# Optimization experiments

Hardware: AMD Instinct MI355X
Metric: run time of the kernel (lower is better)

Reference implementation:

```python
import jax, jax.numpy as jnp
import numpy as np

WS = 8  # window_size

def conv2d(x, w, b, padding=0, dilation=1, groups=1):
    out = jax.lax.conv_general_dilated(
        x, w, window_strides=(1, 1),
        padding=[(padding, padding), (padding, padding)],
        rhs_dilation=(dilation, dilation),
        feature_group_count=groups)
    return out + b[None, :, None, None]

def lrelu(x):
    return jnp.where(x >= 0, x, 0.1 * x)

def ln_cf(x, w, b, eps=1e-6):
    # LayerNorm, channels_first: normalize over channel dim per pixel
    u = x.mean(1, keepdims=True)
    s = ((x - u) ** 2).mean(1, keepdims=True)
    x = (x - u) / jnp.sqrt(s + eps)
    return w[None, :, None, None] * x + b[None, :, None, None]

def window_part(x, ws):
    # b c (h dh) (w dw) -> b (h w) (dh dw c)
    b, c, H, W = x.shape
    h, w = H // ws, W // ws
    x = x.reshape(b, c, h, ws, w, ws).transpose(0, 2, 4, 3, 5, 1)
    return x.reshape(b, h * w, ws * ws * c)

def window_rev(x, ws, H, W, c):
    # b (h w) (dh dw c) -> b c (h dh) (w dw)
    b = x.shape[0]
    h, w = H // ws, W // ws
    x = x.reshape(b, h, w, ws, ws, c).transpose(0, 5, 1, 3, 2, 4)
    return x.reshape(b, c, H, W)

def setup_inputs() -> dict:
    key = jax.random.key(0)
    B, C, H, W = 4, 64, 256, 256
    ws = WS
    E = ws * ws * C  # 4096
    ks = iter(jax.random.split(key, 40))
    def rn(shape, scale=1.0):
        return jax.random.normal(next(ks), shape, jnp.float32) * scale
    z = lambda *s: jnp.zeros(s, jnp.float32)
    d = {}
    d['x'] = rn((B, C, H, W))
    d['Wv'] = rn((C, C, 1, 1), C ** -0.5); d['bv'] = z(C)
    d['Wri'] = rn((C // 4, C, 1, 1), C ** -0.5); d['bri'] = z(C // 4)
    d['Wrc'] = rn((C // 4, C, 1, 1), C ** -0.5); d['brc'] = z(C // 4)
    d['ln_w'] = jnp.ones((C // 4,), jnp.float32); d['ln_b'] = z(C // 4)
    d['Wca'] = rn((C, C // 4, 1, 1), (C // 4) ** -0.5); d['bca'] = z(C)
    d['Wsa'] = rn((1, C // 4, 3, 3), (9 * C // 4) ** -0.5); d['bsa'] = z(1)
    d['Wm1'] = rn((E // 2, E), E ** -0.5); d['bm1'] = z(E // 2)
    d['Wm2'] = rn((E, E // 2), (E // 2) ** -0.5); d['bm2'] = z(E)
    d['Wq'] = rn((C, C), C ** -0.5); d['bq'] = z(C)
    d['Wk'] = rn((C, C), C ** -0.5); d['bk'] = z(C)
    d['Wd1'] = rn((C, 1, 3, 3), 1.0 / 3.0); d['bd1'] = z(C)
    d['Wd2'] = rn((C, 1, 3, 3), 1.0 / 3.0); d['bd2'] = z(C)
    d['Wo'] = rn((C, C, 1, 1), C ** -0.5); d['bo'] = z(C)
    return d

def reference(x, Wv, bv, Wri, bri, Wrc, brc, ln_w, ln_b, Wca, bca, Wsa, bsa,
              Wm1, bm1, Wm2, bm2, Wq, bq, Wk, bk, Wd1, bd1, Wd2, bd2, Wo, bo):
    B, C, H, W = x.shape
    ws = WS
    E = ws * ws * C
    v = conv2d(x, Wv, bv)
    # ---- MaskPre (route) ----
    x1 = lrelu(conv2d(v, Wri, bri))                       # [B,C/4,H,W]
    x_ = lrelu(ln_cf(conv2d(v, Wrc, brc), ln_w, ln_b))    # [B,C/4,H,W]
    ca = jax.nn.sigmoid(conv2d(x_.mean((2, 3), keepdims=True), Wca, bca))  # [B,C,1,1]
    sa = jax.nn.sigmoid(conv2d(x_, Wsa, bsa, padding=1))                   # [B,1,H,W]
    xm = window_part(x1.mean(1, keepdims=True), ws)       # [B,N,ws^2]
    var_x = jnp.var(xm, axis=-1, ddof=1)                  # torch.var is unbiased
    N = var_x.shape[1]
    k_top = N // 2
    _, idx = jax.lax.top_k(-var_x, k_top)                 # k smallest-variance windows
    mask_bin = jnp.ones((B, N), x.dtype).at[jnp.arange(B)[:, None], idx].set(0.0)
    m = jnp.broadcast_to(mask_bin[:, :, None], (B, N, E))
    m = lrelu(m @ Wm1.T + bm1)
    mask = m @ Wm2.T + bm2                                # [B,N,E]
    # ---- windowed attention / skip split ----
    vs = v * sa
    vw = window_part(v, ws)                               # [B,N,ws^2*C]
    vsw = window_part(vs, ws)
    qkw = window_part(jnp.concatenate([x, x], axis=1), ws)  # [B,N,ws^2*2C]
    v1 = vw * mask
    v2 = vsw * (1.0 - mask)
    mask_qk = jnp.concatenate(
        [mask.reshape(B, N, ws * ws, C)] * 2, axis=-1).reshape(B, N, ws * ws * 2 * C)
    qk1 = (qkw * mask_qk).reshape(B, N * ws * ws, 2 * C)
    q1 = (qk1[..., :C] @ Wq.T + bq).reshape(B * N, ws * ws, C)
    k1 = (qk1[..., C:] @ Wk.T + bk).reshape(B * N, ws * ws, C)
    v1r = v1.reshape(B * N, ws * ws, C)
    attn = jax.nn.softmax(q1 @ jnp.swapaxes(k1, -1, -2), axis=-1)  # [BN,ws^2,ws^2]
    f_attn = (attn @ v1r).reshape(B, N, ws * ws * C)
    attn_out = f_attn + v2
    out = window_rev(attn_out, ws, H, W, C)               # [B,C,H,W]
    # ---- spatial conv branch + projections ----
    c1 = conv2d(out, Wd1, bd1, padding=1, groups=C)
    c2 = conv2d(c1, Wd2, bd2, padding=2, dilation=2, groups=C)
    out = jax.nn.gelu(c2, approximate=False) * ca + out
    out = conv2d(out, Wo, bo)
    return out
```

## Files before the change

### kernel.cpp

```cpp
#include <hip/hip_runtime.h>
#include <hip/hip_bf16.h>
#include <math.h>

typedef __attribute__((ext_vector_type(8))) short short8;
typedef __attribute__((ext_vector_type(16))) float f32x16;

__device__ __forceinline__ float lrelu(float x){ return x >= 0.f ? x : 0.1f*x; }
__device__ __forceinline__ float sigmoidf(float x){ return 1.f/(1.f+expf(-x)); }
__device__ __forceinline__ short f2bf(float f){
  __hip_bfloat16 hb = __float2bfloat16(f);
  return *reinterpret_cast<short*>(&hb);
}
__device__ __forceinline__ float bf16f(short s){
  return __uint_as_float(((unsigned)(unsigned short)s)<<16);
}

__global__ void k0_combine(const float* __restrict__ Wv, const float* __restrict__ bv,
                           const float* __restrict__ Wri, const float* __restrict__ bri,
                           const float* __restrict__ Wrc, const float* __restrict__ brc,
                           float* __restrict__ WriE, float* __restrict__ briE,
                           float* __restrict__ WrcE, float* __restrict__ brcE){
  int idx = blockIdx.x*256 + threadIdx.x;
  if (idx < 1024){
    int j = idx>>6, c = idx&63;
    float s1=0.f, s2=0.f;
    for (int k=0;k<64;k++){ s1 = fmaf(Wri[j*64+k], Wv[k*64+c], s1); s2 = fmaf(Wrc[j*64+k], Wv[k*64+c], s2); }
    WriE[idx]=s1; WrcE[idx]=s2;
  }
  if (idx < 16){
    float s1=bri[idx], s2=brc[idx];
    for (int k=0;k<64;k++){ s1 = fmaf(Wri[idx*64+k], bv[k], s1); s2 = fmaf(Wrc[idx*64+k], bv[k], s2); }
    briE[idx]=s1; brcE[idx]=s2;
  }
}

__global__ void k_prep(const float* __restrict__ Wq, const float* __restrict__ Wk,
                       const float* __restrict__ Wo, const float* __restrict__ Wv,
                       const float* __restrict__ WriE, const float* __restrict__ WrcE,
                       const float* __restrict__ bq, const float* __restrict__ bk,
                       float* __restrict__ WoT, float* __restrict__ WT,
                       short* __restrict__ WFrag){
  int idx = blockIdx.x*256 + threadIdx.x;
  if (idx < 4096){
    int oc = idx>>6, c = idx&63;
    WoT[(c<<6)|oc] = Wo[idx];
    WT[c*96 + oc] = Wv[idx];
  } else if (idx < 6144){
    int t = idx - 4096;
    int j = (t>>6) & 15, c = t & 63;
    if (t < 1024) WT[c*96 + 64 + j] = WriE[j*64+c];
    else          WT[c*96 + 80 + j] = WrcE[j*64+c];
  }
  if (idx < 2560){
    int w = idx / 1280;
    int r1 = idx - w*1280;
    int part = r1 / 640;
    int r2 = r1 - part*640;
    int mt = r2 / 320;
    int r3 = r2 - mt*320;
    int kt = r3 >> 6;
    int lane = r3 & 63;
    const float* W = w ? Wk : Wq;
    const float* B = w ? bk : bq;
    int j = (mt<<5) | (lane & 31);
    int hh = lane >> 5;
    short8 frag;
    #pragma unroll
    for (int i=0;i<8;i++){
      int kl = (hh<<2) + (i&3) + ((i>>2)<<3);
      float val;
      if (kt < 4) val = W[j*64 + (kt<<4) + kl];
      else        val = (kl==0) ? B[j] : 0.f;
      short hi = f2bf(val);
      frag[i] = part ? f2bf(val - bf16f(hi)) : hi;
    }
    *(short8*)&WFrag[idx<<3] = frag;
  }
}

__global__ void k_premask1(const float* __restrict__ Wm1, const float* __restrict__ bm1,
                           float* __restrict__ mrow1, float* __restrict__ mrow0){
  __shared__ float red[256];
  int j = blockIdx.x, tid = threadIdx.x;
  const float* row = Wm1 + (size_t)j*4096;
  float s=0.f;
  for (int e=tid;e<4096;e+=256) s += row[e];
  red[tid]=s; __syncthreads();
  for (int o=128;o;o>>=1){ if (tid<o) red[tid]+=red[tid+o]; __syncthreads(); }
  if (tid==0){
    float t = red[0]+bm1[j];
    mrow1[j] = lrelu(t);
    mrow0[j] = lrelu(bm1[j]);
  }
}

__global__ void k_premask2(const float* __restrict__ Wm2, const float* __restrict__ bm2,
                           const float* __restrict__ mrow1, const float* __restrict__ mrow0,
                           float* __restrict__ mask1, float* __restrict__ mask0,
                           float* __restrict__ mask1T, float* __restrict__ mask0T){
  __shared__ float r1[256], r0[256];
  int e = blockIdx.x, tid = threadIdx.x;
  const float* row = Wm2 + (size_t)e*2048;
  float s1=0.f, s0=0.f;
  for (int j=tid;j<2048;j+=256){ float wv=row[j]; s1 = fmaf(wv, mrow1[j], s1); s0 = fmaf(wv, mrow0[j], s0); }
  r1[tid]=s1; r0[tid]=s0; __syncthreads();
  for (int o=128;o;o>>=1){ if (tid<o){ r1[tid]+=r1[tid+o]; r0[tid]+=r0[tid+o]; } __syncthreads(); }
  if (tid==0){
    float m1 = r1[0]+bm2[e], m0 = r0[0]+bm2[e];
    mask1[e]=m1; mask0[e]=m0;
    int p = e>>6, c = e&63;
    mask1T[(c<<6)|p]=m1; mask0T[(c<<6)|p]=m0;
  }
}

__global__ __launch_bounds__(256) void k1_pw(
    const float* __restrict__ x, const float* __restrict__ WT,
    const float* __restrict__ bv,
    const float* __restrict__ briE, const float* __restrict__ brcE,
    const float* __restrict__ ln_w, const float* __restrict__ ln_b,
    float* __restrict__ v, float* __restrict__ x_, float* __restrict__ xm,
    float* __restrict__ bsum){
  __shared__ float wred[4][16];
  int tid = threadIdx.x;
  int b = blockIdx.x >> 8;
  int hw = ((blockIdx.x & 255) << 8) | tid;
  const float* xb = x + (((size_t)b)<<22) + hw;
  float acc[64], r1[16], rc[16];
  #pragma unroll
  for (int oc=0;oc<64;oc++) acc[oc]=0.f;
  #pragma unroll
  for (int j=0;j<16;j++){ r1[j]=0.f; rc[j]=0.f; }
  for (int c=0;c<64;c++){
    float xv = xb[((size_t)c)<<16];
    const float* wrow = WT + c*96;
    #pragma unroll
    for (int oc=0;oc<64;oc++) acc[oc] = fmaf(wrow[oc], xv, acc[oc]);
    #pragma unroll
    for (int j=0;j<16;j++){ r1[j] = fmaf(wrow[64+j], xv, r1[j]); rc[j] = fmaf(wrow[80+j], xv, rc[j]); }
  }
  float* vb = v + (((size_t)b)<<22) + hw;
  #pragma unroll
  for (int oc=0;oc<64;oc++) vb[((size_t)oc)<<16] = acc[oc] + bv[oc];
  float s1=0.f;
  #pragma unroll
  for (int j=0;j<16;j++){ float t = r1[j]+briE[j]; s1 += lrelu(t); }
  xm[(((size_t)b)<<16)+hw] = s1*(1.f/16.f);
  float u=0.f;
  #pragma unroll
  for (int j=0;j<16;j++){ rc[j] += brcE[j]; u += rc[j]; }
  u *= (1.f/16.f);
  float s2=0.f;
  #pragma unroll
  for (int j=0;j<16;j++){ float d = rc[j]-u; s2 += d*d; }
  float inv = 1.0f / sqrtf(s2*(1.f/16.f) + 1e-6f);
  float xs[16];
  #pragma unroll
  for (int j=0;j<16;j++){
    float t = (rc[j]-u)*inv*ln_w[j] + ln_b[j];
    t = lrelu(t);
    xs[j]=t;
    x_[(((size_t)(b*16+j))<<16)+hw] = t;
  }
  int lane = tid & 63, wv_ = tid >> 6;
  #pragma unroll
  for (int j=0;j<16;j++){
    float val = xs[j];
    for (int o=32;o;o>>=1) val += __shfl_down(val, o, 64);
    if (lane==0) wred[wv_][j]=val;
  }
  __syncthreads();
  if (tid<16) bsum[blockIdx.x*16+tid] = wred[0][tid]+wred[1][tid]+wred[2][tid]+wred[3][tid];
}

__global__ __launch_bounds__(256) void k2_sa(const float* __restrict__ x_,
    const float* __restrict__ Wsa, const float* __restrict__ bsa, float* __restrict__ sa){
  int idx = blockIdx.x*256 + threadIdx.x;
  int b = idx>>16; int hw = idx & 65535; int h = hw>>8, wcol = hw & 255;
  float acc = bsa[0];
  for (int ch=0; ch<16; ++ch){
    const float* plane = x_ + (((size_t)(b*16+ch))<<16);
    #pragma unroll
    for (int ky=0;ky<3;ky++){
      int y = h + ky - 1;
      if ((unsigned)y >= 256u) continue;
      #pragma unroll
      for (int kx=0;kx<3;kx++){
        int xx = wcol + kx - 1;
        if ((unsigned)xx >= 256u) continue;
        acc = fmaf(Wsa[ch*9+ky*3+kx], plane[(y<<8)+xx], acc);
      }
    }
  }
  sa[idx] = sigmoidf(acc);
}

__global__ void k3_ca(const float* __restrict__ bsum, const float* __restrict__ Wca,
                      const float* __restrict__ bca, float* __restrict__ ca){
  __shared__ float meanx[4][16];
  int tid = threadIdx.x;
  if (tid < 64){
    int b = tid>>4, j = tid&15;
    float s=0.f;
    for (int blk=0;blk<256;blk++) s += bsum[(b*256+blk)*16 + j];
    meanx[b][j] = s*(1.f/65536.f);
  }
  __syncthreads();
  int b = tid>>6, oc = tid&63;
  float a = bca[oc];
  #pragma unroll
  for (int j=0;j<16;j++) a = fmaf(Wca[oc*16+j], meanx[b][j], a);
  ca[tid] = sigmoidf(a);
}

__global__ void k4a_var(const float* __restrict__ xm, float* __restrict__ var){
  int t = blockIdx.x*256 + threadIdx.x;
  int b = t>>10, n = t&1023, wh = n>>5, ww = n&31;
  const float* base = xm + (((size_t)b)<<16) + (wh<<11) + (ww<<3);
  float s=0.f;
  #pragma unroll
  for (int dh=0;dh<8;dh++){
    #pragma unroll
    for (int dw=0;dw<8;dw++) s += base[(dh<<8)+dw];
  }
  float mean = s*(1.f/64.f);
  float ss=0.f;
  #pragma unroll
  for (int dh=0;dh<8;dh++){
    #pragma unroll
    for (int dw=0;dw<8;dw++){ float d = base[(dh<<8)+dw]-mean; ss += d*d; }
  }
  var[t] = ss*(1.f/63.f);
}

__global__ __launch_bounds__(1024) void k4b_sel(const float* __restrict__ var, float* __restrict__ sel){
  __shared__ float vs[1024];
  int b = blockIdx.x, tid = threadIdx.x;
  float mine = var[b*1024+tid];
  vs[tid]=mine; __syncthreads();
  int rank=0;
  for (int j=0;j<1024;j++){
    float o = vs[j];
    rank += (o < mine) || (o == mine && j < tid);
  }
  sel[b*1024+tid] = (rank >= 512) ? 1.f : 0.f;
}

__global__ __launch_bounds__(256, 2) void k6_attn(
    const float* __restrict__ x, const float* __restrict__ v, const float* __restrict__ sa,
    const float* __restrict__ sel,
    const float* __restrict__ mask1, const float* __restrict__ mask0,
    const float* __restrict__ mask1T, const float* __restrict__ mask0T,
    const short* __restrict__ WFrag,
    float* __restrict__ out){
  __shared__ short8 QBlds[4][16][64];
  int tid = threadIdx.x;
  int lane = tid & 63, wvi = tid >> 6;
  int l31 = lane & 31, h = lane >> 5;
  int bid = blockIdx.x;
  int blk = ((bid & 7) << 7) | (bid >> 3);
  int wg = (blk << 2) | wvi;
  int b = wg >> 10, n = wg & 1023;
  int pix0 = ((n >> 5) << 11) | ((n & 31) << 3);
  bool sel1 = sel[wg] > 0.5f;
  const float* mrow  = sel1 ? mask1  : mask0;
  const float* mrowT = sel1 ? mask1T : mask0T;
  size_t cbase = (((size_t)b) << 22) + pix0;

  short8 XBh[2][4], XBl[2][4];
  #pragma unroll
  for (int nt=0;nt<2;nt++){
    int p = (nt<<5) | l31;
    size_t gp = cbase + ((size_t)((p>>3)<<8)) + (p&7);
    const float* mr = mrow + (p<<6);
    #pragma unroll
    for (int kt=0;kt<4;kt++){
      float4 ma = *(const float4*)&mr[(kt<<4)+(h<<2)];
      float4 mb = *(const float4*)&mr[(kt<<4)+(h<<2)+8];
      float xv[8];
      #pragma unroll
      for (int i=0;i<8;i++){
        int c = (kt<<4) + (h<<2) + (i&3) + ((i>>2)<<3);
        xv[i] = x[gp + ((size_t)c<<16)];
      }
      xv[0]*=ma.x; xv[1]*=ma.y; xv[2]*=ma.z; xv[3]*=ma.w;
      xv[4]*=mb.x; xv[5]*=mb.y; xv[6]*=mb.z; xv[7]*=mb.w;
      short8 fh, fl;
      #pragma unroll
      for (int i=0;i<8;i++){
        short hi = f2bf(xv[i]); fh[i]=hi; fl[i]=f2bf(xv[i]-bf16f(hi));
      }
      XBh[nt][kt]=fh; XBl[nt][kt]=fl;
    }
  }
  short8 CB;
  #pragma unroll
  for (int i=0;i<8;i++) CB[i]=0;
  CB[0] = h ? (short)0 : (short)0x3F80;

  #pragma unroll
  for (int mt=0;mt<2;mt++){
    short8 WAh[5], WAl[5];
    #pragma unroll
    for (int kt=0;kt<5;kt++){
      WAh[kt] = *(const short8*)&WFrag[(((0*2+0)*2+mt)*5+kt)*512 + (lane<<3)];
      WAl[kt] = *(const short8*)&WFrag[(((0*2+1)*2+mt)*5+kt)*512 + (lane<<3)];
    }
    #pragma unroll
    for (int nt=0;nt<2;nt++){
      f32x16 acc;
      #pragma unroll
      for (int r=0;r<16;r++) acc[r]=0.f;
      #pragma unroll
      for (int kt=0;kt<4;kt++){
        acc = __builtin_amdgcn_mfma_f32_32x32x16_bf16(WAh[kt], XBh[nt][kt], acc, 0,0,0);
        acc = __builtin_amdgcn_mfma_f32_32x32x16_bf16(WAh[kt], XBl[nt][kt], acc, 0,0,0);
        acc = __builtin_amdgcn_mfma_f32_32x32x16_bf16(WAl[kt], XBh[nt][kt], acc, 0,0,0);
      }
      acc = __builtin_amdgcn_mfma_f32_32x32x16_bf16(WAh[4], CB, acc, 0,0,0);
      acc = __builtin_amdgcn_mfma_f32_32x32x16_bf16(WAl[4], CB, acc, 0,0,0);
      short8 fh0, fh1, fl0, fl1;
      #pragma unroll
      for (int i=0;i<8;i++){
        short hi0 = f2bf(acc[i]);   fh0[i]=hi0; fl0[i]=f2bf(acc[i]-bf16f(hi0));
        short hi1 = f2bf(acc[8+i]); fh1[i]=hi1; fl1[i]=f2bf(acc[8+i]-bf16f(hi1));
      }
      QBlds[wvi][(2*mt  )*2+nt][lane] = fh0;
      QBlds[wvi][(2*mt+1)*2+nt][lane] = fh1;
      QBlds[wvi][8+(2*mt  )*2+nt][lane] = fl0;
      QBlds[wvi][8+(2*mt+1)*2+nt][lane] = fl1;
    }
  }

  short8 KAh[2][4], KAl[2][4];
  #pragma unroll
  for (int mt=0;mt<2;mt++){
    short8 WAh[5], WAl[5];
    #pragma unroll
    for (int kt=0;kt<5;kt++){
      WAh[kt] = *(const short8*)&WFrag[(((1*2+0)*2+mt)*5+kt)*512 + (lane<<3)];
      WAl[kt] = *(const short8*)&WFrag[(((1*2+1)*2+mt)*5+kt)*512 + (lane<<3)];
    }
    #pragma unroll
    for (int nt=0;nt<2;nt++){
      f32x16 acc;
      #pragma unroll
      for (int r=0;r<16;r++) acc[r]=0.f;
      #pragma unroll
      for (int kt=0;kt<4;kt++){
        acc = __builtin_amdgcn_mfma_f32_32x32x16_bf16(WAh[kt], XBh[nt][kt], acc, 0,0,0);
        acc = __builtin_amdgcn_mfma_f32_32x32x16_bf16(WAh[kt], XBl[nt][kt], acc, 0,0,0);
        acc = __builtin_amdgcn_mfma_f32_32x32x16_bf16(WAl[kt], XBh[nt][kt], acc, 0,0,0);
      }
      acc = __builtin_amdgcn_mfma_f32_32x32x16_bf16(WAh[4], CB, acc, 0,0,0);
      acc = __builtin_amdgcn_mfma_f32_32x32x16_bf16(WAl[4], CB, acc, 0,0,0);
      #pragma unroll
      for (int i=0;i<8;i++){
        short hi0 = f2bf(acc[i]);   KAh[nt][2*mt  ][i]=hi0; KAl[nt][2*mt  ][i]=f2bf(acc[i]-bf16f(hi0));
        short hi1 = f2bf(acc[8+i]); KAh[nt][2*mt+1][i]=hi1; KAl[nt][2*mt+1][i]=f2bf(acc[8+i]-bf16f(hi1));
      }
    }
  }

  f32x16 ST[2][2];
  #pragma unroll
  for (int nt=0;nt<2;nt++){
    short8 qh[4], ql[4];
    #pragma unroll
    for (int kt=0;kt<4;kt++){
      qh[kt] = QBlds[wvi][kt*2+nt][lane];
      ql[kt] = QBlds[wvi][8+kt*2+nt][lane];
    }
    #pragma unroll
    for (int mt=0;mt<2;mt++){
      f32x16 acc;
      #pragma unroll
      for (int r=0;r<16;r++) acc[r]=0.f;
      #pragma unroll
      for (int kt=0;kt<4;kt++){
        acc = __builtin_amdgcn_mfma_f32_32x32x16_bf16(KAh[mt][kt], qh[kt], acc, 0,0,0);
        acc = __builtin_amdgcn_mfma_f32_32x32x16_bf16(KAh[mt][kt], ql[kt], acc, 0,0,0);
        acc = __builtin_amdgcn_mfma_f32_32x32x16_bf16(KAl[mt][kt], qh[kt], acc, 0,0,0);
      }
      ST[mt][nt] = acc;
    }
  }

  #pragma unroll
  for (int nt=0;nt<2;nt++){
    float mx = ST[0][nt][0];
    #pragma unroll
    for (int r=1;r<16;r++) mx = fmaxf(mx, ST[0][nt][r]);
    #pragma unroll
    for (int r=0;r<16;r++) mx = fmaxf(mx, ST[1][nt][r]);
    mx = fmaxf(mx, __shfl_xor(mx, 32));
    float sum = 0.f;
    #pragma unroll
    for (int mt=0;mt<2;mt++)
      #pragma unroll
      for (int r=0;r<16;r++){ float e = expf(ST[mt][nt][r]-mx); ST[mt][nt][r]=e; sum += e; }
    sum += __shfl_xor(sum, 32);
    float inv = 1.f/sum;
    #pragma unroll
    for (int mt=0;mt<2;mt++)
      #pragma unroll
      for (int r=0;r<16;r++) ST[mt][nt][r] *= inv;
  }

  short8 PB[4][2];
  #pragma unroll
  for (int mt=0;mt<2;mt++)
    #pragma unroll
    for (int nt=0;nt<2;nt++){
      #pragma unroll
      for (int i=0;i<8;i++){
        PB[2*mt  ][nt][i] = f2bf(ST[mt][nt][i]);
        PB[2*mt+1][nt][i] = f2bf(ST[mt][nt][8+i]);
      }
    }

  short8 VA[2][4];
  #pragma unroll
  for (int mt=0;mt<2;mt++){
    int c = (mt<<5) | l31;
    const float* vp = v + cbase + ((size_t)c<<16);
    const float* mTr = mrowT + (c<<6);
    #pragma unroll
    for (int kt=0;kt<4;kt++){
      float4 va = *(const float4*)&vp[((kt<<1)<<8) + (h<<2)];
      float4 vb2 = *(const float4*)&vp[(((kt<<1)|1)<<8) + (h<<2)];
      float4 ma = *(const float4*)&mTr[(kt<<4)+(h<<2)];
      float4 mb = *(const float4*)&mTr[(kt<<4)+(h<<2)+8];
      short8 f;
      f[0]=f2bf(va.x*ma.x); f[1]=f2bf(va.y*ma.y); f[2]=f2bf(va.z*ma.z); f[3]=f2bf(va.w*ma.w);
      f[4]=f2bf(vb2.x*mb.x); f[5]=f2bf(vb2.y*mb.y); f[6]=f2bf(vb2.z*mb.z); f[7]=f2bf(vb2.w*mb.w);
      VA[mt][kt]=f;
    }
  }

  f32x16 FT[2][2];
  #pragma unroll
  for (int mt=0;mt<2;mt++)
    #pragma unroll
    for (int nt=0;nt<2;nt++){
      f32x16 acc;
      #pragma unroll
      for (int r=0;r<16;r++) acc[r]=0.f;
      #pragma unroll
      for (int kt=0;kt<4;kt++)
        acc = __builtin_amdgcn_mfma_f32_32x32x16_bf16(VA[mt][kt], PB[kt][nt], acc, 0,0,0);
      FT[mt][nt] = acc;
    }

  #pragma unroll
  for (int nt=0;nt<2;nt++){
    int p = (nt<<5) | l31;
    int po = ((p>>3)<<8) | (p&7);
    float sav = sa[(((size_t)b)<<16) + pix0 + po];
    const float* mr = mrow + (p<<6);
    #pragma unroll
    for (int mt=0;mt<2;mt++){
      #pragma unroll
      for (int rr=0;rr<4;rr++){
        float4 m4 = *(const float4*)&mr[(mt<<5)+(rr<<3)+(h<<2)];
        #pragma unroll
        for (int t=0;t<4;t++){
          int c = (mt<<5)+(rr<<3)+(h<<2)+t;
          size_t g = cbase + ((size_t)c<<16) + po;
          float vv = v[g];
          float mm = (t==0)?m4.x:(t==1)?m4.y:(t==2)?m4.z:m4.w;
          out[g] = FT[mt][nt][rr*4+t] + sav*vv*(1.f-mm);
        }
      }
    }
  }
}

__global__ __launch_bounds__(256) void k7_fused(const float* __restrict__ in,
    const float* __restrict__ Wd1, const float* __restrict__ bd1,
    const float* __restrict__ Wd2, const float* __restrict__ bd2,
    const float* __restrict__ ca, float* __restrict__ dwout){
  __shared__ float IN[22*23];
  __shared__ float C1[20*21];
  int blk = blockIdx.x;
  int tx = blk & 15, ty = (blk>>4) & 15, ch = (blk>>8) & 63, b = blk>>14;
  int x0 = tx<<4, y0 = ty<<4;
  const float* plane = in + (((size_t)(b*64+ch))<<16);
  int tid = threadIdx.x;
  for (int e = tid; e < 484; e += 256){
    int r = e/22, cc = e - r*22;
    int y = y0 + r - 3, xx = x0 + cc - 3;
    float vv = 0.f;
    if ((unsigned)y < 256u && (unsigned)xx < 256u) vv = plane[(y<<8)+xx];
    IN[r*23+cc] = vv;
  }
  __syncthreads();
  float w1[9], w2[9];
  #pragma unroll
  for (int t=0;t<9;t++){ w1[t]=Wd1[ch*9+t]; w2[t]=Wd2[ch*9+t]; }
  float b1 = bd1[ch];
  for (int e = tid; e < 400; e += 256){
    int r = e/20, cc = e - r*20;
    int yc1 = y0 + r - 2, xc1 = x0 + cc - 2;
    float acc = 0.f;
    if ((unsigned)yc1 < 256u && (unsigned)xc1 < 256u){
      acc = b1;
      #pragma unroll
      for (int ky=0;ky<3;ky++)
        #pragma unroll
        for (int kx=0;kx<3;kx++)
          acc = fmaf(w1[ky*3+kx], IN[(r+ky)*23 + cc+kx], acc);
    }
    C1[r*21+cc] = acc;
  }
  __syncthreads();
  int px = tid & 15, py = tid >> 4;
  float acc = bd2[ch];
  #pragma unroll
  for (int ky=0;ky<3;ky++)
    #pragma unroll
    for (int kx=0;kx<3;kx++)
      acc = fmaf(w2[ky*3+kx], C1[(py+2*ky)*21 + px+2*kx], acc);
  float g = 0.5f*acc*(1.f + erff(acc*0.70710678118654752f));
  float resid = IN[(py+3)*23 + px+3];
  size_t o = (((size_t)(b*64+ch))<<16) + ((size_t)((y0+py)<<8)) + x0+px;
  dwout[o] = fmaf(g, ca[b*64+ch], resid);
}

__global__ __launch_bounds__(256) void k7c_proj(const float* __restrict__ in,
    const float* __restrict__ WoT, const float* __restrict__ bo, float* __restrict__ out){
  int b = blockIdx.x >> 8;
  int hw = ((blockIdx.x & 255) << 8) | threadIdx.x;
  const float* pb = in + (((size_t)b)<<22) + hw;
  float acc[64];
  #pragma unroll
  for (int oc=0;oc<64;oc++) acc[oc]=bo[oc];
  for (int c=0;c<64;c++){
    float xv = pb[((size_t)c)<<16];
    const float* wrow = WoT + (c<<6);
    #pragma unroll
    for (int oc=0;oc<64;oc++) acc[oc] = fmaf(wrow[oc], xv, acc[oc]);
  }
  float* ob = out + (((size_t)b)<<22) + hw;
  #pragma unroll
  for (int oc=0;oc<64;oc++) ob[((size_t)oc)<<16] = acc[oc];
}

extern "C" void kernel_launch(void* const* d_in, const int* in_sizes, int n_in,
                              void* d_out, int out_size, void* d_ws, size_t ws_size,
                              hipStream_t stream) {
  const float* x    = (const float*)d_in[0];
  const float* Wv   = (const float*)d_in[1];
  const float* bv   = (const float*)d_in[2];
  const float* Wri  = (const float*)d_in[3];
  const float* bri  = (const float*)d_in[4];
  const float* Wrc  = (const float*)d_in[5];
  const float* brc  = (const float*)d_in[6];
  const float* ln_w = (const float*)d_in[7];
  const float* ln_b = (const float*)d_in[8];
  const float* Wca  = (const float*)d_in[9];
  const float* bca  = (const float*)d_in[10];
  const float* Wsa  = (const float*)d_in[11];
  const float* bsa  = (const float*)d_in[12];
  const float* Wm1  = (const float*)d_in[13];
  const float* bm1  = (const float*)d_in[14];
  const float* Wm2  = (const float*)d_in[15];
  const float* bm2  = (const float*)d_in[16];
  const float* Wq   = (const float*)d_in[17];
  const float* bq   = (const float*)d_in[18];
  const float* Wk   = (const float*)d_in[19];
  const float* bk   = (const float*)d_in[20];
  const float* Wd1  = (const float*)d_in[21];
  const float* bd1  = (const float*)d_in[22];
  const float* Wd2  = (const float*)d_in[23];
  const float* bd2  = (const float*)d_in[24];
  const float* Wo   = (const float*)d_in[25];
  const float* bo   = (const float*)d_in[26];
  float* out = (float*)d_out;

  float* ws = (float*)d_ws;
  float* v_buf   = ws;
  float* out_buf = v_buf + 16777216;
  float* x_buf   = out_buf + 16777216;
  float* xm_buf  = x_buf + 4194304;
  float* sa_buf  = xm_buf + 262144;
  float* bsum    = sa_buf + 262144;
  float* ca_buf  = bsum + 16384;
  float* var_buf = ca_buf + 256;
  float* sel_buf = var_buf + 4096;
  float* mrow1   = sel_buf + 4096;
  float* mrow0   = mrow1 + 2048;
  float* mask1   = mrow0 + 2048;
  float* mask0   = mask1 + 4096;
  float* mask1T  = mask0 + 4096;
  float* mask0T  = mask1T + 4096;
  float* WoT     = mask0T + 4096;
  float* WT      = WoT + 4096;
  float* WriE    = WT + 6144;
  float* WrcE    = WriE + 1024;
  float* briE    = WrcE + 1024;
  float* brcE    = briE + 16;
  short* WFrag   = (short*)(brcE + 16);
  float* dw_buf  = v_buf;

  k0_combine<<<4,256,0,stream>>>(Wv,bv,Wri,bri,Wrc,brc,WriE,briE,WrcE,brcE);
  k_prep<<<24,256,0,stream>>>(Wq,Wk,Wo,Wv,WriE,WrcE,bq,bk,WoT,WT,WFrag);
  k_premask1<<<2048,256,0,stream>>>(Wm1,bm1,mrow1,mrow0);
  k_premask2<<<4096,256,0,stream>>>(Wm2,bm2,mrow1,mrow0,mask1,mask0,mask1T,mask0T);
  k1_pw<<<1024,256,0,stream>>>(x,WT,bv,briE,brcE,ln_w,ln_b,v_buf,x_buf,xm_buf,bsum);
  k2_sa<<<1024,256,0,stream>>>(x_buf,Wsa,bsa,sa_buf);
  k3_ca<<<1,256,0,stream>>>(bsum,Wca,bca,ca_buf);
  k4a_var<<<16,256,0,stream>>>(xm_buf,var_buf);
  k4b_sel<<<4,1024,0,stream>>>(var_buf,sel_buf);
  k6_attn<<<1024,256,0,stream>>>(x,v_buf,sa_buf,sel_buf,mask1,mask0,mask1T,mask0T,WFrag,out_buf);
  k7_fused<<<65536,256,0,stream>>>(out_buf,Wd1,bd1,Wd2,bd2,ca_buf,dw_buf);
  k7c_proj<<<1024,256,0,stream>>>(dw_buf,WoT,bo,out);
}
```

Before: 393.5 us.

## Move output projection to split-bf16 MFMA and split attention windows across two waves

```diff
diff --git a/kernel.cpp b/kernel.cpp
--- a/kernel.cpp
+++ b/kernel.cpp
@@ -13,6 +13,12 @@
 }
 __device__ __forceinline__ float bf16f(short s){
   return __uint_as_float(((unsigned)(unsigned short)s)<<16);
+}
+
+#define WF(w,part,mt,kt) ((((w)*8 + (part)*4 + (mt)*... 0)
+#undef WF
+__device__ __forceinline__ int WFofs(int w,int part,int mt,int kt){
+  return (((w*2+part)*2+mt)*4+kt)*512;
 }
 
 __global__ void k0_combine(const float* __restrict__ Wv, const float* __restrict__ bv,
@@ -37,13 +43,10 @@
 __global__ void k_prep(const float* __restrict__ Wq, const float* __restrict__ Wk,
                        const float* __restrict__ Wo, const float* __restrict__ Wv,
                        const float* __restrict__ WriE, const float* __restrict__ WrcE,
-                       const float* __restrict__ bq, const float* __restrict__ bk,
-                       float* __restrict__ WoT, float* __restrict__ WT,
-                       short* __restrict__ WFrag){
+                       float* __restrict__ WT, short* __restrict__ WFrag){
   int idx = blockIdx.x*256 + threadIdx.x;
   if (idx < 4096){
     int oc = idx>>6, c = idx&63;
-    WoT[(c<<6)|oc] = Wo[idx];
     WT[c*96 + oc] = Wv[idx];
   } else if (idx < 6144){
     int t = idx - 4096;
@@ -51,30 +54,21 @@
     if (t < 1024) WT[c*96 + 64 + j] = WriE[j*64+c];
     else          WT[c*96 + 80 + j] = WrcE[j*64+c];
   }
-  if (idx < 2560){
-    int w = idx / 1280;
-    int r1 = idx - w*1280;
-    int part = r1 / 640;
-    int r2 = r1 - part*640;
-    int mt = r2 / 320;
-    int r3 = r2 - mt*320;
-    int kt = r3 >> 6;
-    int lane = r3 & 63;
-    const float* W = w ? Wk : Wq;
-    const float* B = w ? bk : bq;
-    int j = (mt<<5) | (lane & 31);
-    int hh = lane >> 5;
+  if (idx < 3072){
+    int w = idx>>10, rem = idx&1023;
+    int part = rem>>9, mt = (rem>>8)&1, kt = (rem>>6)&3, lane = rem&63;
+    const float* W = (w==0)?Wq:((w==1)?Wk:Wo);
+    int j = (mt<<5)|(lane&31);
+    int hh = lane>>5;
     short8 frag;
     #pragma unroll
     for (int i=0;i<8;i++){
       int kl = (hh<<2) + (i&3) + ((i>>2)<<3);
-      float val;
-      if (kt < 4) val = W[j*64 + (kt<<4) + kl];
-      else        val = (kl==0) ? B[j] : 0.f;
+      float val = W[j*64 + (kt<<4) + kl];
       short hi = f2bf(val);
       frag[i] = part ? f2bf(val - bf16f(hi)) : hi;
     }
-    *(short8*)&WFrag[idx<<3] = frag;
+    *(short8*)&WFrag[WFofs(w,part,mt,kt) + (lane<<3)] = frag;
   }
 }
 
@@ -245,20 +239,22 @@
   sel[b*1024+tid] = (rank >= 512) ? 1.f : 0.f;
 }
 
-__global__ __launch_bounds__(256, 2) void k6_attn(
+__global__ __launch_bounds__(256, 3) void k6_attn(
     const float* __restrict__ x, const float* __restrict__ v, const float* __restrict__ sa,
     const float* __restrict__ sel,
     const float* __restrict__ mask1, const float* __restrict__ mask0,
     const float* __restrict__ mask1T, const float* __restrict__ mask0T,
     const short* __restrict__ WFrag,
+    const float* __restrict__ bq, const float* __restrict__ bk,
     float* __restrict__ out){
-  __shared__ short8 QBlds[4][16][64];
+  __shared__ short8 KAlds[2][2][8][64];
   int tid = threadIdx.x;
   int lane = tid & 63, wvi = tid >> 6;
+  int wi = wvi >> 1, ht = wvi & 1;
   int l31 = lane & 31, h = lane >> 5;
   int bid = blockIdx.x;
-  int blk = ((bid & 7) << 7) | (bid >> 3);
-  int wg = (blk << 2) | wvi;
+  int blk = ((bid & 7) << 8) | (bid >> 3);
+  int wg = (blk << 1) | wi;
   int b = wg >> 10, n = wg & 1023;
   int pix0 = ((n >> 5) << 11) | ((n & 31) << 3);
   bool sel1 = sel[wg] > 0.5f;
@@ -266,210 +262,168 @@
   const float* mrowT = sel1 ? mask1T : mask0T;
   size_t cbase = (((size_t)b) << 22) + pix0;
 
-  short8 XBh[2][4], XBl[2][4];
-  #pragma unroll
-  for (int nt=0;nt<2;nt++){
-    int p = (nt<<5) | l31;
-    size_t gp = cbase + ((size_t)((p>>3)<<8)) + (p&7);
-    const float* mr = mrow + (p<<6);
+  int p = (ht<<5) | l31;
+  int po = ((p>>3)<<8) | (p&7);
+  size_t gp = cbase + po;
+  const float* mr = mrow + (p<<6);
+  short8 XBh[4], XBl[4];
+  #pragma unroll
+  for (int kt=0;kt<4;kt++){
+    float4 ma = *(const float4*)&mr[(kt<<4)+(h<<2)];
+    float4 mb = *(const float4*)&mr[(kt<<4)+(h<<2)+8];
+    float xv[8];
+    #pragma unroll
+    for (int i=0;i<8;i++){
+      int c = (kt<<4) + (h<<2) + (i&3) + ((i>>2)<<3);
+      xv[i] = x[gp + ((size_t)c<<16)];
+    }
+    xv[0]*=ma.x; xv[1]*=ma.y; xv[2]*=ma.z; xv[3]*=ma.w;
+    xv[4]*=mb.x; xv[5]*=mb.y; xv[6]*=mb.z; xv[7]*=mb.w;
+    short8 fh, fl;
+    #pragma unroll
+    for (int i=0;i<8;i++){
+      short hi = f2bf(xv[i]); fh[i]=hi; fl[i]=f2bf(xv[i]-bf16f(hi));
+    }
+    XBh[kt]=fh; XBl[kt]=fl;
+  }
+
+  short8 QBh[4], QBl[4];
+  #pragma unroll
+  for (int mt=0;mt<2;mt++){
+    f32x16 acc;
+    #pragma unroll
+    for (int r=0;r<16;r++) acc[r]=0.f;
     #pragma unroll
     for (int kt=0;kt<4;kt++){
-      float4 ma = *(const float4*)&mr[(kt<<4)+(h<<2)];
-      float4 mb = *(const float4*)&mr[(kt<<4)+(h<<2)+8];
-      float xv[8];
+      short8 WAh = *(const short8*)&WFrag[WFofs(0,0,mt,kt) + (lane<<3)];
+      short8 WAl = *(const short8*)&WFrag[WFofs(0,1,mt,kt) + (lane<<3)];
+      acc = __builtin_amdgcn_mfma_f32_32x32x16_bf16(WAh, XBh[kt], acc, 0,0,0);
+      acc = __builtin_amdgcn_mfma_f32_32x32x16_bf16(WAh, XBl[kt], acc, 0,0,0);
+      acc = __builtin_amdgcn_mfma_f32_32x32x16_bf16(WAl, XBh[kt], acc, 0,0,0);
+    }
+    #pragma unroll
+    for (int rr=0;rr<4;rr++){
+      float4 b4 = *(const float4*)&bq[(mt<<5)+(rr<<3)+(h<<2)];
+      acc[4*rr+0]+=b4.x; acc[4*rr+1]+=b4.y; acc[4*rr+2]+=b4.z; acc[4*rr+3]+=b4.w;
+    }
+    #pragma unroll
+    for (int kk=0;kk<2;kk++){
+      short8 fh, fl;
       #pragma unroll
       for (int i=0;i<8;i++){
-        int c = (kt<<4) + (h<<2) + (i&3) + ((i>>2)<<3);
-        xv[i] = x[gp + ((size_t)c<<16)];
-      }
-      xv[0]*=ma.x; xv[1]*=ma.y; xv[2]*=ma.z; xv[3]*=ma.w;
-      xv[4]*=mb.x; xv[5]*=mb.y; xv[6]*=mb.z; xv[7]*=mb.w;
+        float vv = acc[8*kk+i];
+        short hi = f2bf(vv); fh[i]=hi; fl[i]=f2bf(vv-bf16f(hi));
+      }
+      QBh[2*mt+kk]=fh; QBl[2*mt+kk]=fl;
+    }
+  }
+
+  #pragma unroll
+  for (int mt=0;mt<2;mt++){
+    f32x16 acc;
+    #pragma unroll
+    for (int r=0;r<16;r++) acc[r]=0.f;
+    #pragma unroll
+    for (int kt=0;kt<4;kt++){
+      short8 WAh = *(const short8*)&WFrag[WFofs(1,0,mt,kt) + (lane<<3)];
+      short8 WAl = *(const short8*)&WFrag[WFofs(1,1,mt,kt) + (lane<<3)];
+      acc = __builtin_amdgcn_mfma_f32_32x32x16_bf16(WAh, XBh[kt], acc, 0,0,0);
+      acc = __builtin_amdgcn_mfma_f32_32x32x16_bf16(WAh, XBl[kt], acc, 0,0,0);
+      acc = __builtin_amdgcn_mfma_f32_32x32x16_bf16(WAl, XBh[kt], acc, 0,0,0);
+    }
+    #pragma unroll
+    for (int rr=0;rr<4;rr++){
+      float4 b4 = *(const float4*)&bk[(mt<<5)+(rr<<3)+(h<<2)];
+      acc[4*rr+0]+=b4.x; acc[4*rr+1]+=b4.y; acc[4*rr+2]+=b4.z; acc[4*rr+3]+=b4.w;
+    }
+    #pragma unroll
+    for (int kk=0;kk<2;kk++){
       short8 fh, fl;
       #pragma unroll
       for (int i=0;i<8;i++){
-        short hi = f2bf(xv[i]); fh[i]=hi; fl[i]=f2bf(xv[i]-bf16f(hi));
-      }
-      XBh[nt][kt]=fh; XBl[nt][kt]=fl;
-    }
-  }
-  short8 CB;
-  #pragma unroll
-  for (int i=0;i<8;i++) CB[i]=0;
-  CB[0] = h ? (short)0 : (short)0x3F80;
-
+        float vv = acc[8*kk+i];
+        short hi = f2bf(vv); fh[i]=hi; fl[i]=f2bf(vv-bf16f(hi));
+      }
+      KAlds[wi][ht][2*mt+kk][lane]   = fh;
+      KAlds[wi][ht][4+2*mt+kk][lane] = fl;
+    }
+  }
+  __syncthreads();
+
+  f32x16 ST[2];
   #pragma unroll
   for (int mt=0;mt<2;mt++){
-    short8 WAh[5], WAl[5];
-    #pragma unroll
-    for (int kt=0;kt<5;kt++){
-      WAh[kt] = *(const short8*)&WFrag[(((0*2+0)*2+mt)*5+kt)*512 + (lane<<3)];
-      WAl[kt] = *(const short8*)&WFrag[(((0*2+1)*2+mt)*5+kt)*512 + (lane<<3)];
-    }
-    #pragma unroll
-    for (int nt=0;nt<2;nt++){
-      f32x16 acc;
-      #pragma unroll
-      for (int r=0;r<16;r++) acc[r]=0.f;
-      #pragma unroll
-      for (int kt=0;kt<4;kt++){
-        acc = __builtin_amdgcn_mfma_f32_32x32x16_bf16(WAh[kt], XBh[nt][kt], acc, 0,0,0);
-        acc = __builtin_amdgcn_mfma_f32_32x32x16_bf16(WAh[kt], XBl[nt][kt], acc, 0,0,0);
-        acc = __builtin_amdgcn_mfma_f32_32x32x16_bf16(WAl[kt], XBh[nt][kt], acc, 0,0,0);
-      }
-      acc = __builtin_amdgcn_mfma_f32_32x32x16_bf16(WAh[4], CB, acc, 0,0,0);
-      acc = __builtin_amdgcn_mfma_f32_32x32x16_bf16(WAl[4], CB, acc, 0,0,0);
-      short8 fh0, fh1, fl0, fl1;
-      #pragma unroll
-      for (int i=0;i<8;i++){
-        short hi0 = f2bf(acc[i]);   fh0[i]=hi0; fl0[i]=f2bf(acc[i]-bf16f(hi0));
-        short hi1 = f2bf(acc[8+i]); fh1[i]=hi1; fl1[i]=f2bf(acc[8+i]-bf16f(hi1));
-      }
-      QBlds[wvi][(2*mt  )*2+nt][lane] = fh0;
-      QBlds[wvi][(2*mt+1)*2+nt][lane] = fh1;
-      QBlds[wvi][8+(2*mt  )*2+nt][lane] = fl0;
-      QBlds[wvi][8+(2*mt+1)*2+nt][lane] = fl1;
-    }
-  }
-
-  short8 KAh[2][4], KAl[2][4];
-  #pragma unroll
-  for (int mt=0;mt<2;mt++){
-    short8 WAh[5], WAl[5];
-    #pragma unroll
-    for (int kt=0;kt<5;kt++){
-      WAh[kt] = *(const short8*)&WFrag[(((1*2+0)*2+mt)*5+kt)*512 + (lane<<3)];
-      WAl[kt] = *(const short8*)&WFrag[(((1*2+1)*2+mt)*5+kt)*512 + (lane<<3)];
-    }
-    #pragma unroll
-    for (int nt=0;nt<2;nt++){
-      f32x16 acc;
-      #pragma unroll
-      for (int r=0;r<16;r++) acc[r]=0.f;
-      #pragma unroll
-      for (int kt=0;kt<4;kt++){
-        acc = __builtin_amdgcn_mfma_f32_32x32x16_bf16(WAh[kt], XBh[nt][kt], acc, 0,0,0);
-        acc = __builtin_amdgcn_mfma_f32_32x32x16_bf16(WAh[kt], XBl[nt][kt], acc, 0,0,0);
-        acc = __builtin_amdgcn_mfma_f32_32x32x16_bf16(WAl[kt], XBh[nt][kt], acc, 0,0,0);
-      }
-      acc = __builtin_amdgcn_mfma_f32_32x32x16_bf16(WAh[4], CB, acc, 0,0,0);
-      acc = __builtin_amdgcn_mfma_f32_32x32x16_bf16(WAl[4], CB, acc, 0,0,0);
-      #pragma unroll
-      for (int i=0;i<8;i++){
-        short hi0 = f2bf(acc[i]);   KAh[nt][2*mt  ][i]=hi0; KAl[nt][2*mt  ][i]=f2bf(acc[i]-bf16f(hi0));
-        short hi1 = f2bf(acc[8+i]); KAh[nt][2*mt+1][i]=hi1; KAl[nt][2*mt+1][i]=f2bf(acc[8+i]-bf16f(hi1));
-      }
-    }
-  }
-
-  f32x16 ST[2][2];
-  #pragma unroll
-  for (int nt=0;nt<2;nt++){
-    short8 qh[4], ql[4];
+    f32x16 acc;
+    #pragma unroll
+    for (int r=0;r<16;r++) acc[r]=0.f;
     #pragma unroll
     for (int kt=0;kt<4;kt++){
-      qh[kt] = QBlds[wvi][kt*2+nt][lane];
-      ql[kt] = QBlds[wvi][8+kt*2+nt][lane];
-    }
-    #pragma unroll
-    for (int mt=0;mt<2;mt++){
-      f32x16 acc;
-      #pragma unroll
-      for (int r=0;r<16;r++) acc[r]=0.f;
-      #pragma unroll
-      for (int kt=0;kt<4;kt++){
-        acc = __builtin_amdgcn_mfma_f32_32x32x16_bf16(KAh[mt][kt], qh[kt], acc, 0,0,0);
-        acc = __builtin_amdgcn_mfma_f32_32x32x16_bf16(KAh[mt][kt], ql[kt], acc, 0,0,0);
-        acc = __builtin_amdgcn_mfma_f32_32x32x16_bf16(KAl[mt][kt], qh[kt], acc, 0,0,0);
-      }
-      ST[mt][nt] = acc;
-    }
-  }
-
-  #pragma unroll
-  for (int nt=0;nt<2;nt++){
-    float mx = ST[0][nt][0];
-    #pragma unroll
-    for (int r=1;r<16;r++) mx = fmaxf(mx, ST[0][nt][r]);
-    #pragma unroll
-    for (int r=0;r<16;r++) mx = fmaxf(mx, ST[1][nt][r]);
-    mx = fmaxf(mx, __shfl_xor(mx, 32));
-    float sum = 0.f;
-    #pragma unroll
-    for (int mt=0;mt<2;mt++)
-      #pragma unroll
-      for (int r=0;r<16;r++){ float e = expf(ST[mt][nt][r]-mx); ST[mt][nt][r]=e; sum += e; }
-    sum += __shfl_xor(sum, 32);
-    float inv = 1.f/sum;
-    #pragma unroll
-    for (int mt=0;mt<2;mt++)
-      #pragma unroll
-      for (int r=0;r<16;r++) ST[mt][nt][r] *= inv;
-  }
-
-  short8 PB[4][2];
+      short8 kh = KAlds[wi][mt][kt][lane];
+      short8 kl = KAlds[wi][mt][4+kt][lane];
+      acc = __builtin_amdgcn_mfma_f32_32x32x16_bf16(kh, QBh[kt], acc, 0,0,0);
+      acc = __builtin_amdgcn_mfma_f32_32x32x16_bf16(kh, QBl[kt], acc, 0,0,0);
+      acc = __builtin_amdgcn_mfma_f32_32x32x16_bf16(kl, QBh[kt], acc, 0,0,0);
+    }
+    ST[mt] = acc;
+  }
+
+  float mx = ST[0][0];
+  #pragma unroll
+  for (int r=1;r<16;r++) mx = fmaxf(mx, ST[0][r]);
+  #pragma unroll
+  for (int r=0;r<16;r++) mx = fmaxf(mx, ST[1][r]);
+  mx = fmaxf(mx, __shfl_xor(mx, 32));
+  float sum = 0.f;
   #pragma unroll
   for (int mt=0;mt<2;mt++)
     #pragma unroll
-    for (int nt=0;nt<2;nt++){
-      #pragma unroll
-      for (int i=0;i<8;i++){
-        PB[2*mt  ][nt][i] = f2bf(ST[mt][nt][i]);
-        PB[2*mt+1][nt][i] = f2bf(ST[mt][nt][8+i]);
-      }
-    }
-
-  short8 VA[2][4];
-  #pragma unroll
-  for (int mt=0;mt<2;mt++){
-    int c = (mt<<5) | l31;
-    const float* vp = v + cbase + ((size_t)c<<16);
-    const float* mTr = mrowT + (c<<6);
+    for (int r=0;r<16;r++){ float e = expf(ST[mt][r]-mx); ST[mt][r]=e; sum += e; }
+  sum += __shfl_xor(sum, 32);
+  float inv = 1.f/sum;
+
+  short8 PB[4];
+  #pragma unroll
+  for (int mt=0;mt<2;mt++)
+    #pragma unroll
+    for (int kk=0;kk<2;kk++){
+      short8 f;
+      #pragma unroll
+      for (int i=0;i<8;i++) f[i] = f2bf(ST[mt][8*kk+i]*inv);
+      PB[2*mt+kk]=f;
+    }
+
+  float sav = sa[(((size_t)b)<<16) + pix0 + po];
+
+  #pragma unroll
+  for (int mtc=0;mtc<2;mtc++){
+    int c0 = (mtc<<5);
+    int cl = c0 | l31;
+    const float* vp = v + cbase + ((size_t)cl<<16);
+    const float* mTr = mrowT + (cl<<6);
+    f32x16 acc;
+    #pragma unroll
+    for (int r=0;r<16;r++) acc[r]=0.f;
     #pragma unroll
     for (int kt=0;kt<4;kt++){
-      float4 va = *(const float4*)&vp[((kt<<1)<<8) + (h<<2)];
+      float4 va  = *(const float4*)&vp[((kt<<1)<<8) + (h<<2)];
       float4 vb2 = *(const float4*)&vp[(((kt<<1)|1)<<8) + (h<<2)];
       float4 ma = *(const float4*)&mTr[(kt<<4)+(h<<2)];
       float4 mb = *(const float4*)&mTr[(kt<<4)+(h<<2)+8];
       short8 f;
       f[0]=f2bf(va.x*ma.x); f[1]=f2bf(va.y*ma.y); f[2]=f2bf(va.z*ma.z); f[3]=f2bf(va.w*ma.w);
       f[4]=f2bf(vb2.x*mb.x); f[5]=f2bf(vb2.y*mb.y); f[6]=f2bf(vb2.z*mb.z); f[7]=f2bf(vb2.w*mb.w);
-      VA[mt][kt]=f;
-    }
-  }
-
-  f32x16 FT[2][2];
-  #pragma unroll
-  for (int mt=0;mt<2;mt++)
-    #pragma unroll
-    for (int nt=0;nt<2;nt++){
-      f32x16 acc;
-      #pragma unroll
-      for (int r=0;r<16;r++) acc[r]=0.f;
-      #pragma unroll
-      for (int kt=0;kt<4;kt++)
-        acc = __builtin_amdgcn_mfma_f32_32x32x16_bf16(VA[mt][kt], PB[kt][nt], acc, 0,0,0);
-      FT[mt][nt] = acc;
-    }
-
-  #pragma unroll
-  for (int nt=0;nt<2;nt++){
-    int p = (nt<<5) | l31;
-    int po = ((p>>3)<<8) | (p&7);
-    float sav = sa[(((size_t)b)<<16) + pix0 + po];
-    const float* mr = mrow + (p<<6);
-    #pragma unroll
-    for (int mt=0;mt<2;mt++){
-      #pragma unroll
-      for (int rr=0;rr<4;rr++){
-        float4 m4 = *(const float4*)&mr[(mt<<5)+(rr<<3)+(h<<2)];
-        #pragma unroll
-        for (int t=0;t<4;t++){
-          int c = (mt<<5)+(rr<<3)+(h<<2)+t;
-          size_t g = cbase + ((size_t)c<<16) + po;
-          float vv = v[g];
-          float mm = (t==0)?m4.x:(t==1)?m4.y:(t==2)?m4.z:m4.w;
-          out[g] = FT[mt][nt][rr*4+t] + sav*vv*(1.f-mm);
-        }
+      acc = __builtin_amdgcn_mfma_f32_32x32x16_bf16(f, PB[kt], acc, 0,0,0);
+    }
+    #pragma unroll
+    for (int rr=0;rr<4;rr++){
+      float4 m4 = *(const float4*)&mr[c0+(rr<<3)+(h<<2)];
+      #pragma unroll
+      for (int t=0;t<4;t++){
+        int c = c0 + (rr<<3) + (h<<2) + t;
+        size_t g = cbase + ((size_t)c<<16) + po;
+        float vv = v[g];
+        float mm = (t==0)?m4.x:(t==1)?m4.y:(t==2)?m4.z:m4.w;
+        out[g] = acc[4*rr+t] + sav*vv*(1.f-mm);
       }
     }
   }
@@ -526,23 +480,60 @@
   dwout[o] = fmaf(g, ca[b*64+ch], resid);
 }
 
-__global__ __launch_bounds__(256) void k7c_proj(const float* __restrict__ in,
-    const float* __restrict__ WoT, const float* __restrict__ bo, float* __restrict__ out){
-  int b = blockIdx.x >> 8;
-  int hw = ((blockIdx.x & 255) << 8) | threadIdx.x;
-  const float* pb = in + (((size_t)b)<<22) + hw;
-  float acc[64];
-  #pragma unroll
-  for (int oc=0;oc<64;oc++) acc[oc]=bo[oc];
-  for (int c=0;c<64;c++){
-    float xv = pb[((size_t)c)<<16];
-    const float* wrow = WoT + (c<<6);
-    #pragma unroll
-    for (int oc=0;oc<64;oc++) acc[oc] = fmaf(wrow[oc], xv, acc[oc]);
-  }
-  float* ob = out + (((size_t)b)<<22) + hw;
-  #pragma unroll
-  for (int oc=0;oc<64;oc++) ob[((size_t)oc)<<16] = acc[oc];
+__global__ __launch_bounds__(256, 3) void k7c_proj(const float* __restrict__ in,
+    const short* __restrict__ WFrag, const float* __restrict__ bo,
+    float* __restrict__ out){
+  int tid = threadIdx.x;
+  int lane = tid & 63, wvi = tid >> 6;
+  int l31 = lane & 31, h = lane >> 5;
+  int blk = blockIdx.x;
+  int b = blk >> 8;
+  int hw0 = ((blk & 255) << 8) | (wvi << 6);
+  size_t base = ((size_t)b) << 22;
+  #pragma unroll
+  for (int nt=0;nt<2;nt++){
+    int px = hw0 | (nt<<5) | l31;
+    short8 XH[4], XL[4];
+    #pragma unroll
+    for (int kt=0;kt<4;kt++){
+      float xv[8];
+      #pragma unroll
+      for (int i=0;i<8;i++){
+        int c = (kt<<4) + (h<<2) + (i&3) + ((i>>2)<<3);
+        xv[i] = in[base + ((size_t)c<<16) + px];
+      }
+      short8 fh, fl;
+      #pragma unroll
+      for (int i=0;i<8;i++){
+        short hi = f2bf(xv[i]); fh[i]=hi; fl[i]=f2bf(xv[i]-bf16f(hi));
+      }
+      XH[kt]=fh; XL[kt]=fl;
+    }
+    #pragma unroll
+    for (int mt=0;mt<2;mt++){
+      f32x16 acc;
+      #pragma unroll
+      for (int r=0;r<16;r++) acc[r]=0.f;
+      #pragma unroll
+      for (int kt=0;kt<4;kt++){
+        short8 WAh = *(const short8*)&WFrag[WFofs(2,0,mt,kt) + (lane<<3)];
+        short8 WAl = *(const short8*)&WFrag[WFofs(2,1,mt,kt) + (lane<<3)];
+        acc = __builtin_amdgcn_mfma_f32_32x32x16_bf16(WAh, XH[kt], acc, 0,0,0);
+        acc = __builtin_amdgcn_mfma_f32_32x32x16_bf16(WAh, XL[kt], acc, 0,0,0);
+        acc = __builtin_amdgcn_mfma_f32_32x32x16_bf16(WAl, XH[kt], acc, 0,0,0);
+      }
+      #pragma unroll
+      for (int rr=0;rr<4;rr++){
+        float4 b4 = *(const float4*)&bo[(mt<<5)+(rr<<3)+(h<<2)];
+        #pragma unroll
+        for (int t=0;t<4;t++){
+          int oc = (mt<<5) + (rr<<3) + (h<<2) + t;
+          float bb = (t==0)?b4.x:(t==1)?b4.y:(t==2)?b4.z:b4.w;
+          out[base + ((size_t)oc<<16) + px] = acc[4*rr+t] + bb;
+        }
+      }
+    }
+  }
 }
 
 extern "C" void kernel_launch(void* const* d_in, const int* in_sizes, int n_in,
@@ -593,8 +584,7 @@
   float* mask0   = mask1 + 4096;
   float* mask1T  = mask0 + 4096;
   float* mask0T  = mask1T + 4096;
-  float* WoT     = mask0T + 4096;
-  float* WT      = WoT + 4096;
+  float* WT      = mask0T + 4096;
   float* WriE    = WT + 6144;
   float* WrcE    = WriE + 1024;
   float* briE    = WrcE + 1024;
@@ -603,7 +593,7 @@
   float* dw_buf  = v_buf;
 
   k0_combine<<<4,256,0,stream>>>(Wv,bv,Wri,bri,Wrc,brc,WriE,briE,WrcE,brcE);
-  k_prep<<<24,256,0,stream>>>(Wq,Wk,Wo,Wv,WriE,WrcE,bq,bk,WoT,WT,WFrag);
+  k_prep<<<24,256,0,stream>>>(Wq,Wk,Wo,Wv,WriE,WrcE,WT,WFrag);
   k_premask1<<<2048,256,0,stream>>>(Wm1,bm1,mrow1,mrow0);
   k_premask2<<<4096,256,0,stream>>>(Wm2,bm2,mrow1,mrow0,mask1,mask0,mask1T,mask0T);
   k1_pw<<<1024,256,0,stream>>>(x,WT,bv,briE,brcE,ln_w,ln_b,v_buf,x_buf,xm_buf,bsum);
@@ -611,7 +601,7 @@
   k3_ca<<<1,256,0,stream>>>(bsum,Wca,bca,ca_buf);
   k4a_var<<<16,256,0,stream>>>(xm_buf,var_buf);
   k4b_sel<<<4,1024,0,stream>>>(var_buf,sel_buf);
-  k6_attn<<<1024,256,0,stream>>>(x,v_buf,sa_buf,sel_buf,mask1,mask0,mask1T,mask0T,WFrag,out_buf);
+  k6_attn<<<2048,256,0,stream>>>(x,v_buf,sa_buf,sel_buf,mask1,mask0,mask1T,mask0T,WFrag,bq,bk,out_buf);
   k7_fused<<<65536,256,0,stream>>>(out_buf,Wd1,bd1,Wd2,bd2,ca_buf,dw_buf);
-  k7c_proj<<<1024,256,0,stream>>>(dw_buf,WoT,bo,out);
-}
+  k7c_proj<<<1024,256,0,stream>>>(dw_buf,WFrag,bo,out);
+}
```

Measured after the change: 393.0 us. About the same (-0.1%).
